# Kernel optimization log

Hardware: AMD Instinct MI355X
Metric: run time of the kernel (lower is better)

Reference implementation:

```python
import jax, jax.numpy as jnp
import numpy as np

NMS_THRE = 0.4
NEG = -1e30  # sentinel for sort key of suppressed boxes


def _iou_adjacency(boxes, nms_thre):
    # boxes: [N,4] in cxcywh -> xyxy, then dense IoU >= thre adjacency (no self loops)
    cx, cy, w, h = boxes[:, 0], boxes[:, 1], boxes[:, 2], boxes[:, 3]
    x1 = cx - w / 2
    y1 = cy - h / 2
    x2 = x1 + w
    y2 = y1 + h
    b = jnp.stack([x1, y1, x2, y2], axis=-1)  # [N,4]
    area = (x2 - x1) * (y2 - y1)
    lt = jnp.maximum(b[:, None, :2], b[None, :, :2])  # [N,N,2]
    rb = jnp.minimum(b[:, None, 2:], b[None, :, 2:])
    wh = jnp.clip(rb - lt, 0.0)
    inter = wh[..., 0] * wh[..., 1]
    iou = inter / (area[:, None] + area[None, :] - inter)
    n = boxes.shape[0]
    return (iou >= nms_thre) & (~jnp.eye(n, dtype=bool))


def _greedy_suppress(valid0, adj, scores):
    # Sequential greedy NMS over candidates in descending score order.
    # valid shrinks monotonically, and valid <= valid0 always, so clearing
    # neighbors via adj row exactly matches the torch loop (which only clears
    # neighbors that were initially valid -- already-false entries are no-ops).
    order = jnp.argsort(-scores)

    def body(k, valid):
        idx = order[k]
        return jnp.where(valid[idx], valid & (~adj[idx]), valid)

    return jax.lax.fori_loop(0, scores.shape[0], body, valid0)


def _per_class(pro_c, con_c, conf_c, adj):
    # scatter_max over adjacency: max of con over neighbors (0 if no neighbors,
    # matching torch_scatter's zero-init)
    adj_con = jnp.max(jnp.where(adj, con_c[None, :], 0.0), axis=1)
    valid0 = (pro_c >= conf_c) & (pro_c >= adj_con) & (pro_c >= con_c)
    return _greedy_suppress(valid0, adj, pro_c)


def _per_image(pro, con, boxes, scale, conf_thres):
    # pro/con: [N,C]; boxes: [N,4] cxcywh; scale: scalar; conf_thres: [C]
    adj = _iou_adjacency(boxes, NMS_THRE)
    survive = jax.vmap(_per_class, in_axes=(1, 1, 0, None))(pro, con, conf_thres, adj)  # [C,N]
    b = boxes * scale
    cx, cy, w, h = b[:, 0], b[:, 1], b[:, 2], b[:, 3]
    xyxy = jnp.stack([cx - 0.5 * w, cy - 0.5 * h, cx + 0.5 * w, cy + 0.5 * h], axis=-1)  # [N,4]
    scores = pro.T  # [C,N]
    C = scores.shape[0]
    bws = jnp.concatenate(
        [jnp.broadcast_to(xyxy[None], (C,) + xyxy.shape), scores[..., None]], axis=-1
    )  # [C,N,5]
    bws = bws * survive[..., None].astype(bws.dtype)  # zero out suppressed rows
    key = jnp.where(survive, scores, NEG)
    perm = jnp.argsort(-key, axis=1)  # per-class descending score order
    bws = jnp.take_along_axis(bws, perm[..., None], axis=1)
    mask = jnp.take_along_axis(survive, perm, axis=1)
    return bws, mask


def setup_inputs() -> dict:
    key = jax.random.key(0)
    k1, k2, k3, k4 = jax.random.split(key, 4)
    B, N, C = 4, 3600, 16
    return {
        "pro_max": jax.random.uniform(k1, (B, N, C), dtype=jnp.float32),
        "con_max": jax.random.uniform(k2, (B, N, C), dtype=jnp.float32),
        "pred_boxes": jax.random.uniform(k3, (B, N, 4), dtype=jnp.float32),
        "image_scales": jax.random.uniform(k4, (B,), dtype=jnp.float32),
        "conf_thres": jnp.zeros((C,), dtype=jnp.float32),
    }


def reference(pro_max, con_max, pred_boxes, image_scales, conf_thres):
    # Returns (boxes_with_scores [B,C,N,5] sorted per class by score desc,
    #          survive_mask [B,C,N] aligned with the sorted rows).
    return jax.vmap(_per_image, in_axes=(0, 0, 0, 0, None))(
        pro_max, con_max, pred_boxes, image_scales, conf_thres
    )
```

## Files before the change

kernel.cpp:

```cpp
#include <hip/hip_runtime.h>
#include <cstdint>

typedef unsigned long long u64;
typedef unsigned int u32;

#define B_ 4
#define N_ 3600
#define C_ 16
#define NW_ 57
#define NPAD_ 3648
#define RPW_ 4
#define RPB_ 16
#define TPI_ 1596
#define HW0_ 1856
#define HW1_ 1792
#define CH_ 64
#define NT_ 512
#define NWV_ 8
#define RPWG_ 8

__global__ __launch_bounds__(256, 4) void k_adj(const float* __restrict__ boxes,
                                                u64* __restrict__ adj) {
#pragma clang fp contract(off)
    __shared__ float4 sbox[HW0_];
    const int tid  = threadIdx.x;
    const int lane = tid & 63;
    const int wv   = tid >> 6;
    const int g    = blockIdx.x;
    const int b    = g / (N_ / RPB_);
    const int rg   = g % (N_ / RPB_);
    const int r0   = rg * RPB_ + wv * RPW_;
    const int w0   = rg >> 2;
    const size_t bN = (size_t)b * N_;

    float4 bi[RPW_];
    float  ai[RPW_];
#pragma unroll
    for (int r = 0; r < RPW_; ++r) {
        const float4 bx = reinterpret_cast<const float4*>(boxes)[bN + r0 + r];
        const float x1 = bx.x - bx.z * 0.5f;
        const float y1 = bx.y - bx.w * 0.5f;
        const float x2 = x1 + bx.z;
        const float y2 = y1 + bx.w;
        bi[r] = make_float4(x1, y1, x2, y2);
        ai[r] = (x2 - x1) * (y2 - y1);
    }
    const double MID = (double)0.4f - 0x1p-26;

    u64 row[RPW_];
#pragma unroll
    for (int r = 0; r < RPW_; ++r) row[r] = 0ull;

    int jbase = 0;
    for (int h = 0; h < 2; ++h) {
        const int cnt  = h ? HW1_ : HW0_;
        const int wlo  = jbase >> 6;
        const int wcnt = cnt >> 6;
        if (w0 < wlo + wcnt) {
            const int tw0 = max(w0 - wlo, 0);
            const int jj0 = tw0 << 6;
            __syncthreads();
            for (int jj = jj0 + tid; jj < cnt; jj += 256) {
                const int j = jbase + jj;
                float x1 = 0.f, y1 = 0.f, x2 = 0.f, y2 = 0.f;
                if (j < N_) {
                    const float4 bx = reinterpret_cast<const float4*>(boxes)[bN + j];
                    x1 = bx.x - bx.z * 0.5f;
                    y1 = bx.y - bx.w * 0.5f;
                    x2 = x1 + bx.z;
                    y2 = y1 + bx.w;
                }
                sbox[jj] = make_float4(x1, y1, x2, y2);
            }
            __syncthreads();

            for (int tw = tw0; tw < wcnt; ++tw) {
                const int tglob = wlo + tw;
                const float4 bj = sbox[tw * 64 + lane];
                const float ajr = (bj.z - bj.x) * (bj.w - bj.y);
#pragma unroll
                for (int r = 0; r < RPW_; ++r) {
                    const float ltx = fmaxf(bi[r].x, bj.x);
                    const float lty = fmaxf(bi[r].y, bj.y);
                    const float rbx = fminf(bi[r].z, bj.z);
                    const float rby = fminf(bi[r].w, bj.w);
                    const float whx = fmaxf(rbx - ltx, 0.0f);
                    const float why = fmaxf(rby - lty, 0.0f);
                    const float inter = whx * why;
                    const float denom = (ai[r] + ajr) - inter;
                    const int pred = ((double)inter > MID * (double)denom);
                    const u64 m = __ballot(pred);
                    if (lane == tglob) row[r] = m;
                }
            }
        }
        jbase += cnt;
    }

#pragma unroll
    for (int r = 0; r < RPW_; ++r)
        if (lane == w0) row[r] &= ~(1ull << ((r0 + r) & 63));

#pragma unroll
    for (int r = 0; r < RPW_; ++r)
        if (lane >= w0 && lane < NW_)
            adj[(bN + r0 + r) * (size_t)NW_ + lane] = row[r];
}

__global__ __launch_bounds__(256) void k_tr(u64* __restrict__ adj,
                                            u32* __restrict__ cnt) {
    if (blockIdx.x == 0) {
        for (int x = threadIdx.x; x < B_ * C_ * 16; x += 256) cnt[x] = 0;
    }
    const int lane = threadIdx.x & 63;
    const int wv   = threadIdx.x >> 6;
    const int p    = blockIdx.x * 4 + wv;
    const int b    = p / TPI_;
    const int p2   = p % TPI_;
    int wi = (int)((1.0f + sqrtf((float)(8 * p2 + 1))) * 0.5f);
    while (wi * (wi - 1) / 2 > p2) --wi;
    while ((wi + 1) * wi / 2 <= p2) ++wi;
    const int wj = p2 - wi * (wi - 1) / 2;
    const size_t bN = (size_t)b * N_;

    u64 x = adj[(bN + wj * 64 + lane) * (size_t)NW_ + wi];

    const u64 M[6] = {0x00000000FFFFFFFFull, 0x0000FFFF0000FFFFull,
                      0x00FF00FF00FF00FFull, 0x0F0F0F0F0F0F0F0Full,
                      0x3333333333333333ull, 0x5555555555555555ull};
#pragma unroll
    for (int si = 0; si < 6; ++si) {
        const int s = 32 >> si;
        const u64 m = M[si];
        const u64 t = __shfl_xor(x, s);
        x = ((lane & s) == 0) ? ((x & m) | ((t & m) << s))
                              : ((x & ~m) | ((t & ~m) >> s));
    }

    const int rowi = wi * 64 + lane;
    if (rowi < N_)
        adj[(bN + rowi) * (size_t)NW_ + wj] = x;
}

__global__ __launch_bounds__(256) void k_acon(const u64* __restrict__ adj,
                                              const float* __restrict__ con,
                                              const float* __restrict__ pro,
                                              const float* __restrict__ conf,
                                              u64* __restrict__ cand,
                                              u32* __restrict__ cnt) {
    const int tid  = threadIdx.x;
    const int lane = tid & 63;
    const int wv   = tid >> 6;
    const int g    = blockIdx.x;
    const int b    = g / (N_ / 4);
    const int i    = (g % (N_ / 4)) * 4 + wv;
    const size_t bN = (size_t)b * N_;

    u64 w = (lane < NW_) ? adj[(bN + i) * (size_t)NW_ + lane] : 0ull;

    float cm[C_];
#pragma unroll
    for (int k = 0; k < C_; ++k) cm[k] = 0.0f;

    while (w) {
        const int bit = __builtin_ctzll(w); w &= w - 1;
        const int j   = lane * 64 + bit;
        const float4* cp = reinterpret_cast<const float4*>(con + (bN + j) * C_);
        const float4 c0 = cp[0], c1 = cp[1], c2 = cp[2], c3 = cp[3];
        cm[0]  = fmaxf(cm[0],  c0.x); cm[1]  = fmaxf(cm[1],  c0.y);
        cm[2]  = fmaxf(cm[2],  c0.z); cm[3]  = fmaxf(cm[3],  c0.w);
        cm[4]  = fmaxf(cm[4],  c1.x); cm[5]  = fmaxf(cm[5],  c1.y);
        cm[6]  = fmaxf(cm[6],  c1.z); cm[7]  = fmaxf(cm[7],  c1.w);
        cm[8]  = fmaxf(cm[8],  c2.x); cm[9]  = fmaxf(cm[9],  c2.y);
        cm[10] = fmaxf(cm[10], c2.z); cm[11] = fmaxf(cm[11], c2.w);
        cm[12] = fmaxf(cm[12], c3.x); cm[13] = fmaxf(cm[13], c3.y);
        cm[14] = fmaxf(cm[14], c3.z); cm[15] = fmaxf(cm[15], c3.w);
    }

#pragma unroll
    for (int off = 1; off < 64; off <<= 1) {
#pragma unroll
        for (int k = 0; k < C_; ++k) cm[k] = fmaxf(cm[k], __shfl_xor(cm[k], off));
    }
    if (lane == 0) {
        const float4* cp = reinterpret_cast<const float4*>(con + (bN + i) * C_);
        const float4 c0 = cp[0], c1 = cp[1], c2 = cp[2], c3 = cp[3];
        const float4* pp = reinterpret_cast<const float4*>(pro + (bN + i) * C_);
        const float4 p0 = pp[0], p1 = pp[1], p2 = pp[2], p3 = pp[3];
        const float4* fp = reinterpret_cast<const float4*>(conf);
        const float4 f0 = fp[0], f1 = fp[1], f2 = fp[2], f3 = fp[3];
        const float th[C_] = {
            fmaxf(cm[0],  c0.x), fmaxf(cm[1],  c0.y),
            fmaxf(cm[2],  c0.z), fmaxf(cm[3],  c0.w),
            fmaxf(cm[4],  c1.x), fmaxf(cm[5],  c1.y),
            fmaxf(cm[6],  c1.z), fmaxf(cm[7],  c1.w),
            fmaxf(cm[8],  c2.x), fmaxf(cm[9],  c2.y),
            fmaxf(cm[10], c2.z), fmaxf(cm[11], c2.w),
            fmaxf(cm[12], c3.x), fmaxf(cm[13], c3.y),
            fmaxf(cm[14], c3.z), fmaxf(cm[15], c3.w)};
        const float pr[C_] = {p0.x, p0.y, p0.z, p0.w, p1.x, p1.y, p1.z, p1.w,
                              p2.x, p2.y, p2.z, p2.w, p3.x, p3.y, p3.z, p3.w};
        const float cf[C_] = {f0.x, f0.y, f0.z, f0.w, f1.x, f1.y, f1.z, f1.w,
                              f2.x, f2.y, f2.z, f2.w, f3.x, f3.y, f3.z, f3.w};
#pragma unroll
        for (int k = 0; k < C_; ++k) {
            if (pr[k] >= cf[k] && pr[k] >= th[k]) {
                const u32 pb = __float_as_uint(pr[k]);
                const u32 pk = pb ^ ((pb >> 31) ? 0xFFFFFFFFu : 0x80000000u);
                const u32 pos = atomicAdd(&cnt[(b * C_ + k) * 16], 1u);
                cand[(size_t)(b * C_ + k) * N_ + pos] =
                    (((u64)(~pk)) << 32) | (u32)i;
            }
        }
    }
}

union OvT {
    u64 keys[NPAD_];
    u64 srows[2][CH_][NW_];
};

__global__ __launch_bounds__(NT_) void k_nms(const u64* __restrict__ cand,
                                             const u32* __restrict__ cnt,
                                             const u64* __restrict__ adj,
                                             const float* __restrict__ boxes,
                                             const float* __restrict__ scales,
                                             float* __restrict__ out) {
#pragma clang fp contract(off)
    __shared__ OvT ov;
    __shared__ u32 sidx[NPAD_];
    __shared__ float sscore[NPAD_];
    __shared__ u64 sintra[CH_];
    __shared__ u64 vmask[NW_];
    __shared__ u64 s_accept;
    __shared__ u32 slist[NPAD_];
    __shared__ float slistf[NPAD_];
    __shared__ u32 s_S;
    const int tid  = threadIdx.x;
    const int lane = tid & 63;
    const int wv   = tid >> 6;
    const int bc   = blockIdx.x;
    const int b    = bc / C_;
    const size_t bN = (size_t)b * N_;

    const int T  = (int)cnt[bc * 16];
    const int TW = (T + 63) >> 6;
    for (int x = tid; x < TW * 64; x += NT_)
        ov.keys[x] = (x < T) ? cand[(size_t)bc * N_ + x] : ~0ull;
    if (tid < NW_) vmask[tid] = 0ull;
    __syncthreads();

    for (int xp = 0; xp * NT_ < T; ++xp) {
        const int x  = xp * NT_ + tid;
        const u64 kx = (x < T) ? ov.keys[x] : ~0ull;
        u32 rank = 0;
        for (int yb = 0; yb < TW; ++yb) {
            const u64 ky = ov.keys[yb * 64 + lane];
            const u32 kyl = (u32)ky, kyh = (u32)(ky >> 32);
#pragma unroll
            for (int l = 0; l < 64; ++l) {
                const u64 kb =
                    ((u64)(u32)__builtin_amdgcn_readlane((int)kyh, l) << 32)
                  |  (u64)(u32)__builtin_amdgcn_readlane((int)kyl, l);
                rank += (kb < kx) ? 1u : 0u;
            }
        }
        if (x < T) {
            const u32 i = (u32)(kx & 0xFFFFFFFFull);
            sidx[rank] = i;
            const u32 pk = ~((u32)(kx >> 32));
            const u32 pb = (pk & 0x80000000u) ? (pk ^ 0x80000000u) : ~pk;
            sscore[rank] = __uint_as_float(pb);
            atomicOr(&vmask[i >> 6], 1ull << (i & 63));
        }
    }
    __syncthreads();

#pragma unroll
    for (int rr = 0; rr < RPWG_; ++rr) {
        const int r = wv * RPWG_ + rr;
        const u32 idx = (r < T) ? sidx[r] : 0u;
        if (lane < NW_) ov.srows[0][r][lane] = adj[(bN + idx) * (size_t)NW_ + lane];
    }
    __syncthreads();

    u32 S = 0;
    const int NCH = (T + CH_ - 1) / CH_;
    for (int ch = 0; ch < NCH; ++ch) {
        const int cur = ch & 1, nxt = cur ^ 1;
        const int c0 = ch * CH_;
        const int cn = min(CH_, T - c0);
        const int havenext = (ch + 1 < NCH);

        u64 pre[RPWG_];
#pragma unroll
        for (int rr = 0; rr < RPWG_; ++rr) {
            const int r = wv * RPWG_ + rr;
            const int q = c0 + CH_ + r;
            const u32 idxn = (havenext && q < T) ? sidx[q] : 0u;
            pre[rr] = (havenext && lane < NW_)
                        ? adj[(bN + idxn) * (size_t)NW_ + lane] : 0ull;
        }
#pragma unroll
        for (int rr = 0; rr < RPWG_; ++rr) {
            const int r = wv * RPWG_ + rr;
            const u32 idxr = (c0 + r < T) ? sidx[c0 + r] : 0u;
            const u64 rj = ov.srows[cur][lane][idxr >> 6];
            const u64 ib = __ballot((lane < cn) && ((rj >> (idxr & 63)) & 1ull));
            if (lane == 0) sintra[r] = ib;
        }
        __syncthreads();

        if (wv == 0) {
            const u32 idxme = (c0 + lane < T) ? sidx[c0 + lane] : 0u;
            const u64 vm = vmask[idxme >> 6];
            u64 cv = __ballot((lane < cn) && ((vm >> (idxme & 63)) & 1ull));
            const u64 iv = sintra[lane];
            const u32 ivLo = (u32)iv, ivHi = (u32)(iv >> 32);
            u64 accept = 0ull;
            while (cv) {
                const int r = __builtin_ctzll(cv);
                accept |= 1ull << r;
                const u64 ir =
                    ((u64)(u32)__builtin_amdgcn_readlane((int)ivHi, r) << 32)
                  |  (u64)(u32)__builtin_amdgcn_readlane((int)ivLo, r);
                cv &= ~(ir | (1ull << r));
            }
            if (lane == 0) s_accept = accept;
            const u32 bitl = (u32)((accept >> lane) & 1ull);
            if (bitl) {
                const u32 pos = S + (u32)__popcll(accept & ((1ull << lane) - 1ull));
                slist[pos]  = idxme;
                slistf[pos] = sscore[c0 + lane];
            }
            S += (u32)__popcll(accept);
        }
        __syncthreads();

        const u64 ac = s_accept;
        u64 acc = 0ull;
#pragma unroll
        for (int rr = 0; rr < RPWG_; ++rr) {
            const int r = wv * RPWG_ + rr;
            if ((ac >> r) & 1ull)
                acc |= ov.srows[cur][r][min(lane, NW_ - 1)];
        }
        if (lane < NW_ && acc)
            atomicAnd(&vmask[lane], ~acc);
        if (havenext) {
#pragma unroll
            for (int rr = 0; rr < RPWG_; ++rr) {
                const int r = wv * RPWG_ + rr;
                if (lane < NW_) ov.srows[nxt][r][lane] = pre[rr];
            }
        }
        __syncthreads();
    }
    if (wv == 0 && lane == 0) s_S = S;
    __syncthreads();

    const int Sf = (int)s_S;
    const float s = scales[b];
    for (int r = tid; r < N_; r += NT_) {
        float o0 = 0.f, o1 = 0.f, o2 = 0.f, o3 = 0.f, o4 = 0.f, mk = 0.f;
        if (r < Sf) {
            const int idx = (int)slist[r];
            const float4 bx = reinterpret_cast<const float4*>(boxes)[bN + idx];
            const float scx = bx.x * s, scy = bx.y * s;
            const float sw  = bx.z * s, sh  = bx.w * s;
            o0 = scx - 0.5f * sw;
            o1 = scy - 0.5f * sh;
            o2 = scx + 0.5f * sw;
            o3 = scy + 0.5f * sh;
            o4 = slistf[r];
            mk = 1.0f;
        }
        float* o = out + ((size_t)bc * N_ + r) * 5;
        o[0] = o0; o[1] = o1; o[2] = o2; o[3] = o3; o[4] = o4;
        out[(size_t)B_ * C_ * N_ * 5 + (size_t)bc * N_ + r] = mk;
    }
}

extern "C" void kernel_launch(void* const* d_in, const int* in_sizes, int n_in,
                              void* d_out, int out_size, void* d_ws, size_t ws_size,
                              hipStream_t stream) {
    const float* pro    = (const float*)d_in[0];
    const float* con    = (const float*)d_in[1];
    const float* boxes  = (const float*)d_in[2];
    const float* scales = (const float*)d_in[3];
    const float* conf   = (const float*)d_in[4];

    char* ws = (char*)d_ws;
    u64* adj = (u64*)ws;
    size_t off = (size_t)B_ * N_ * NW_ * sizeof(u64);
    u64* cand = (u64*)(ws + off);
    off += (size_t)B_ * C_ * N_ * sizeof(u64);
    u32* cnt = (u32*)(ws + off);

    k_adj <<<B_ * N_ / RPB_, 256, 0, stream>>>(boxes, adj);
    k_tr  <<<B_ * TPI_ / 4,  256, 0, stream>>>(adj, cnt);
    k_acon<<<B_ * N_ / 4,    256, 0, stream>>>(adj, con, pro, conf, cand, cnt);
    k_nms <<<B_ * C_,        NT_, 0, stream>>>(cand, cnt, adj, boxes,
                                               scales, (float*)d_out);
}
```

Baseline: 170.7 us.

## Fuse four NMS kernels into one cooperative persistent kernel with grid syncs

Merges the adjacency, transpose, neighbor-max/candidate and greedy NMS kernels into a single cooperative launch of 256 persistent blocks separated by grid.sync, removing launch gaps between stages. The output is pre-zeroed up front so the final stage writes only surviving rows. The intra-chunk greedy acceptance loop now resolves several non-conflicting candidates per iteration using ballot and an OR-reduction instead of one readlane step per candidate. Costs include grid-wide barriers, lower parallelism in the early stages (256 blocks), and only 64 of the 256 blocks doing the serial NMS stage.

Measured after the change: 278.6 us. 1.63x slower.

```diff
diff --git a/kernel.cpp b/kernel.cpp
--- a/kernel.cpp
+++ b/kernel.cpp
@@ -1,5 +1,8 @@
 #include <hip/hip_runtime.h>
+#include <hip/hip_cooperative_groups.h>
 #include <cstdint>
+
+namespace cg = cooperative_groups;
 
 typedef unsigned long long u64;
 typedef unsigned int u32;
@@ -9,8 +12,9 @@
 #define C_ 16
 #define NW_ 57
 #define NPAD_ 3648
-#define RPW_ 4
+#define RPW_ 2
 #define RPB_ 16
+#define NUNITS_ (B_ * N_ / RPB_)
 #define TPI_ 1596
 #define HW0_ 1856
 #define HW1_ 1792
@@ -18,244 +22,257 @@
 #define NT_ 512
 #define NWV_ 8
 #define RPWG_ 8
-
-__global__ __launch_bounds__(256, 4) void k_adj(const float* __restrict__ boxes,
-                                                u64* __restrict__ adj) {
+#define GRID_ 256
+
+union SMem {
+    float4 sbox[HW0_];
+    struct {
+        union {
+            u64 keys[NPAD_];
+            u64 srows[2][CH_][NW_];
+        } ov;
+        u32 sidx[NPAD_];
+        float sscore[NPAD_];
+        u32 slist[NPAD_];
+        float slistf[NPAD_];
+        u64 sintra[CH_];
+        u64 vmask[NW_];
+        u64 s_accept;
+        u32 s_S;
+    } nms;
+};
+
+__global__ void __launch_bounds__(NT_) k_all(const float* __restrict__ pro,
+                                             const float* __restrict__ con,
+                                             const float* __restrict__ boxes,
+                                             const float* __restrict__ scales,
+                                             const float* __restrict__ conf,
+                                             u64* __restrict__ adj,
+                                             u64* __restrict__ cand,
+                                             u32* __restrict__ cnt,
+                                             float* __restrict__ out,
+                                             int nout) {
 #pragma clang fp contract(off)
-    __shared__ float4 sbox[HW0_];
+    __shared__ SMem sm;
+    cg::grid_group grid = cg::this_grid();
     const int tid  = threadIdx.x;
     const int lane = tid & 63;
     const int wv   = tid >> 6;
-    const int g    = blockIdx.x;
-    const int b    = g / (N_ / RPB_);
-    const int rg   = g % (N_ / RPB_);
-    const int r0   = rg * RPB_ + wv * RPW_;
-    const int w0   = rg >> 2;
-    const size_t bN = (size_t)b * N_;
-
-    float4 bi[RPW_];
-    float  ai[RPW_];
-#pragma unroll
-    for (int r = 0; r < RPW_; ++r) {
-        const float4 bx = reinterpret_cast<const float4*>(boxes)[bN + r0 + r];
-        const float x1 = bx.x - bx.z * 0.5f;
-        const float y1 = bx.y - bx.w * 0.5f;
-        const float x2 = x1 + bx.z;
-        const float y2 = y1 + bx.w;
-        bi[r] = make_float4(x1, y1, x2, y2);
-        ai[r] = (x2 - x1) * (y2 - y1);
-    }
+    const int bid  = blockIdx.x;
     const double MID = (double)0.4f - 0x1p-26;
 
-    u64 row[RPW_];
-#pragma unroll
-    for (int r = 0; r < RPW_; ++r) row[r] = 0ull;
-
-    int jbase = 0;
-    for (int h = 0; h < 2; ++h) {
-        const int cnt  = h ? HW1_ : HW0_;
-        const int wlo  = jbase >> 6;
-        const int wcnt = cnt >> 6;
-        if (w0 < wlo + wcnt) {
-            const int tw0 = max(w0 - wlo, 0);
-            const int jj0 = tw0 << 6;
-            __syncthreads();
-            for (int jj = jj0 + tid; jj < cnt; jj += 256) {
-                const int j = jbase + jj;
-                float x1 = 0.f, y1 = 0.f, x2 = 0.f, y2 = 0.f;
-                if (j < N_) {
-                    const float4 bx = reinterpret_cast<const float4*>(boxes)[bN + j];
-                    x1 = bx.x - bx.z * 0.5f;
-                    y1 = bx.y - bx.w * 0.5f;
-                    x2 = x1 + bx.z;
-                    y2 = y1 + bx.w;
+    {
+        float4* o4 = reinterpret_cast<float4*>(out);
+        const int n4 = nout >> 2;
+        const float4 z = make_float4(0.f, 0.f, 0.f, 0.f);
+        for (int x = bid * NT_ + tid; x < n4; x += GRID_ * NT_) o4[x] = z;
+        if (bid == 0)
+            for (int x = tid; x < B_ * C_ * 16; x += NT_) cnt[x] = 0;
+    }
+
+    for (int u = bid; u < NUNITS_; u += GRID_) {
+        const int b  = u / (N_ / RPB_);
+        const int rg = u % (N_ / RPB_);
+        const int r0 = rg * RPB_ + wv * RPW_;
+        const int w0 = rg >> 2;
+        const size_t bN = (size_t)b * N_;
+
+        float4 bi[RPW_];
+        float  ai[RPW_];
+#pragma unroll
+        for (int r = 0; r < RPW_; ++r) {
+            const float4 bx = reinterpret_cast<const float4*>(boxes)[bN + r0 + r];
+            const float x1 = bx.x - bx.z * 0.5f;
+            const float y1 = bx.y - bx.w * 0.5f;
+            const float x2 = x1 + bx.z;
+            const float y2 = y1 + bx.w;
+            bi[r] = make_float4(x1, y1, x2, y2);
+            ai[r] = (x2 - x1) * (y2 - y1);
+        }
+
+        u64 row[RPW_];
+#pragma unroll
+        for (int r = 0; r < RPW_; ++r) row[r] = 0ull;
+
+        int jbase = 0;
+        for (int h = 0; h < 2; ++h) {
+            const int cnt_h = h ? HW1_ : HW0_;
+            const int wlo   = jbase >> 6;
+            const int wcnt  = cnt_h >> 6;
+            if (w0 < wlo + wcnt) {
+                const int tw0 = max(w0 - wlo, 0);
+                const int jj0 = tw0 << 6;
+                __syncthreads();
+                for (int jj = jj0 + tid; jj < cnt_h; jj += NT_) {
+                    const int j = jbase + jj;
+                    float x1 = 0.f, y1 = 0.f, x2 = 0.f, y2 = 0.f;
+                    if (j < N_) {
+                        const float4 bx =
+                            reinterpret_cast<const float4*>(boxes)[bN + j];
+                        x1 = bx.x - bx.z * 0.5f;
+                        y1 = bx.y - bx.w * 0.5f;
+                        x2 = x1 + bx.z;
+                        y2 = y1 + bx.w;
+                    }
+                    sm.sbox[jj] = make_float4(x1, y1, x2, y2);
                 }
-                sbox[jj] = make_float4(x1, y1, x2, y2);
-            }
-            __syncthreads();
-
-            for (int tw = tw0; tw < wcnt; ++tw) {
-                const int tglob = wlo + tw;
-                const float4 bj = sbox[tw * 64 + lane];
-                const float ajr = (bj.z - bj.x) * (bj.w - bj.y);
-#pragma unroll
-                for (int r = 0; r < RPW_; ++r) {
-                    const float ltx = fmaxf(bi[r].x, bj.x);
-                    const float lty = fmaxf(bi[r].y, bj.y);
-                    const float rbx = fminf(bi[r].z, bj.z);
-                    const float rby = fminf(bi[r].w, bj.w);
-                    const float whx = fmaxf(rbx - ltx, 0.0f);
-                    const float why = fmaxf(rby - lty, 0.0f);
-                    const float inter = whx * why;
-                    const float denom = (ai[r] + ajr) - inter;
-                    const int pred = ((double)inter > MID * (double)denom);
-                    const u64 m = __ballot(pred);
-                    if (lane == tglob) row[r] = m;
+                __syncthreads();
+
+                for (int tw = tw0; tw < wcnt; ++tw) {
+                    const int tglob = wlo + tw;
+                    const float4 bj = sm.sbox[tw * 64 + lane];
+                    const float ajr = (bj.z - bj.x) * (bj.w - bj.y);
+#pragma unroll
+                    for (int r = 0; r < RPW_; ++r) {
+                        const float ltx = fmaxf(bi[r].x, bj.x);
+                        const float lty = fmaxf(bi[r].y, bj.y);
+                        const float rbx = fminf(bi[r].z, bj.z);
+                        const float rby = fminf(bi[r].w, bj.w);
+                        const float whx = fmaxf(rbx - ltx, 0.0f);
+                        const float why = fmaxf(rby - lty, 0.0f);
+                        const float inter = whx * why;
+                        const float denom = (ai[r] + ajr) - inter;
+                        const int pred = ((double)inter > MID * (double)denom);
+                        const u64 m = __ballot(pred);
+                        if (lane == tglob) row[r] = m;
+                    }
                 }
             }
-        }
-        jbase += cnt;
-    }
-
-#pragma unroll
-    for (int r = 0; r < RPW_; ++r)
-        if (lane == w0) row[r] &= ~(1ull << ((r0 + r) & 63));
-
-#pragma unroll
-    for (int r = 0; r < RPW_; ++r)
-        if (lane >= w0 && lane < NW_)
-            adj[(bN + r0 + r) * (size_t)NW_ + lane] = row[r];
-}
-
-__global__ __launch_bounds__(256) void k_tr(u64* __restrict__ adj,
-                                            u32* __restrict__ cnt) {
-    if (blockIdx.x == 0) {
-        for (int x = threadIdx.x; x < B_ * C_ * 16; x += 256) cnt[x] = 0;
-    }
-    const int lane = threadIdx.x & 63;
-    const int wv   = threadIdx.x >> 6;
-    const int p    = blockIdx.x * 4 + wv;
-    const int b    = p / TPI_;
-    const int p2   = p % TPI_;
-    int wi = (int)((1.0f + sqrtf((float)(8 * p2 + 1))) * 0.5f);
-    while (wi * (wi - 1) / 2 > p2) --wi;
-    while ((wi + 1) * wi / 2 <= p2) ++wi;
-    const int wj = p2 - wi * (wi - 1) / 2;
-    const size_t bN = (size_t)b * N_;
-
-    u64 x = adj[(bN + wj * 64 + lane) * (size_t)NW_ + wi];
-
-    const u64 M[6] = {0x00000000FFFFFFFFull, 0x0000FFFF0000FFFFull,
-                      0x00FF00FF00FF00FFull, 0x0F0F0F0F0F0F0F0Full,
-                      0x3333333333333333ull, 0x5555555555555555ull};
-#pragma unroll
-    for (int si = 0; si < 6; ++si) {
-        const int s = 32 >> si;
-        const u64 m = M[si];
-        const u64 t = __shfl_xor(x, s);
-        x = ((lane & s) == 0) ? ((x & m) | ((t & m) << s))
-                              : ((x & ~m) | ((t & ~m) >> s));
-    }
-
-    const int rowi = wi * 64 + lane;
-    if (rowi < N_)
-        adj[(bN + rowi) * (size_t)NW_ + wj] = x;
-}
-
-__global__ __launch_bounds__(256) void k_acon(const u64* __restrict__ adj,
-                                              const float* __restrict__ con,
-                                              const float* __restrict__ pro,
-                                              const float* __restrict__ conf,
-                                              u64* __restrict__ cand,
-                                              u32* __restrict__ cnt) {
-    const int tid  = threadIdx.x;
-    const int lane = tid & 63;
-    const int wv   = tid >> 6;
-    const int g    = blockIdx.x;
-    const int b    = g / (N_ / 4);
-    const int i    = (g % (N_ / 4)) * 4 + wv;
-    const size_t bN = (size_t)b * N_;
-
-    u64 w = (lane < NW_) ? adj[(bN + i) * (size_t)NW_ + lane] : 0ull;
-
-    float cm[C_];
-#pragma unroll
-    for (int k = 0; k < C_; ++k) cm[k] = 0.0f;
-
-    while (w) {
-        const int bit = __builtin_ctzll(w); w &= w - 1;
-        const int j   = lane * 64 + bit;
-        const float4* cp = reinterpret_cast<const float4*>(con + (bN + j) * C_);
-        const float4 c0 = cp[0], c1 = cp[1], c2 = cp[2], c3 = cp[3];
-        cm[0]  = fmaxf(cm[0],  c0.x); cm[1]  = fmaxf(cm[1],  c0.y);
-        cm[2]  = fmaxf(cm[2],  c0.z); cm[3]  = fmaxf(cm[3],  c0.w);
-        cm[4]  = fmaxf(cm[4],  c1.x); cm[5]  = fmaxf(cm[5],  c1.y);
-        cm[6]  = fmaxf(cm[6],  c1.z); cm[7]  = fmaxf(cm[7],  c1.w);
-        cm[8]  = fmaxf(cm[8],  c2.x); cm[9]  = fmaxf(cm[9],  c2.y);
-        cm[10] = fmaxf(cm[10], c2.z); cm[11] = fmaxf(cm[11], c2.w);
-        cm[12] = fmaxf(cm[12], c3.x); cm[13] = fmaxf(cm[13], c3.y);
-        cm[14] = fmaxf(cm[14], c3.z); cm[15] = fmaxf(cm[15], c3.w);
-    }
-
-#pragma unroll
-    for (int off = 1; off < 64; off <<= 1) {
-#pragma unroll
-        for (int k = 0; k < C_; ++k) cm[k] = fmaxf(cm[k], __shfl_xor(cm[k], off));
-    }
-    if (lane == 0) {
-        const float4* cp = reinterpret_cast<const float4*>(con + (bN + i) * C_);
-        const float4 c0 = cp[0], c1 = cp[1], c2 = cp[2], c3 = cp[3];
-        const float4* pp = reinterpret_cast<const float4*>(pro + (bN + i) * C_);
-        const float4 p0 = pp[0], p1 = pp[1], p2 = pp[2], p3 = pp[3];
-        const float4* fp = reinterpret_cast<const float4*>(conf);
-        const float4 f0 = fp[0], f1 = fp[1], f2 = fp[2], f3 = fp[3];
-        const float th[C_] = {
-            fmaxf(cm[0],  c0.x), fmaxf(cm[1],  c0.y),
-            fmaxf(cm[2],  c0.z), fmaxf(cm[3],  c0.w),
-            fmaxf(cm[4],  c1.x), fmaxf(cm[5],  c1.y),
-            fmaxf(cm[6],  c1.z), fmaxf(cm[7],  c1.w),
-            fmaxf(cm[8],  c2.x), fmaxf(cm[9],  c2.y),
-            fmaxf(cm[10], c2.z), fmaxf(cm[11], c2.w),
-            fmaxf(cm[12], c3.x), fmaxf(cm[13], c3.y),
-            fmaxf(cm[14], c3.z), fmaxf(cm[15], c3.w)};
-        const float pr[C_] = {p0.x, p0.y, p0.z, p0.w, p1.x, p1.y, p1.z, p1.w,
-                              p2.x, p2.y, p2.z, p2.w, p3.x, p3.y, p3.z, p3.w};
-        const float cf[C_] = {f0.x, f0.y, f0.z, f0.w, f1.x, f1.y, f1.z, f1.w,
-                              f2.x, f2.y, f2.z, f2.w, f3.x, f3.y, f3.z, f3.w};
-#pragma unroll
-        for (int k = 0; k < C_; ++k) {
-            if (pr[k] >= cf[k] && pr[k] >= th[k]) {
-                const u32 pb = __float_as_uint(pr[k]);
-                const u32 pk = pb ^ ((pb >> 31) ? 0xFFFFFFFFu : 0x80000000u);
-                const u32 pos = atomicAdd(&cnt[(b * C_ + k) * 16], 1u);
-                cand[(size_t)(b * C_ + k) * N_ + pos] =
-                    (((u64)(~pk)) << 32) | (u32)i;
-            }
-        }
-    }
-}
-
-union OvT {
-    u64 keys[NPAD_];
-    u64 srows[2][CH_][NW_];
-};
-
-__global__ __launch_bounds__(NT_) void k_nms(const u64* __restrict__ cand,
-                                             const u32* __restrict__ cnt,
-                                             const u64* __restrict__ adj,
-                                             const float* __restrict__ boxes,
-                                             const float* __restrict__ scales,
-                                             float* __restrict__ out) {
-#pragma clang fp contract(off)
-    __shared__ OvT ov;
-    __shared__ u32 sidx[NPAD_];
-    __shared__ float sscore[NPAD_];
-    __shared__ u64 sintra[CH_];
-    __shared__ u64 vmask[NW_];
-    __shared__ u64 s_accept;
-    __shared__ u32 slist[NPAD_];
-    __shared__ float slistf[NPAD_];
-    __shared__ u32 s_S;
-    const int tid  = threadIdx.x;
-    const int lane = tid & 63;
-    const int wv   = tid >> 6;
-    const int bc   = blockIdx.x;
-    const int b    = bc / C_;
+            jbase += cnt_h;
+        }
+
+#pragma unroll
+        for (int r = 0; r < RPW_; ++r)
+            if (lane == w0) row[r] &= ~(1ull << ((r0 + r) & 63));
+#pragma unroll
+        for (int r = 0; r < RPW_; ++r)
+            if (lane >= w0 && lane < NW_)
+                adj[(bN + r0 + r) * (size_t)NW_ + lane] = row[r];
+    }
+
+    grid.sync();
+
+    for (int p = bid * NWV_ + wv; p < B_ * TPI_; p += GRID_ * NWV_) {
+        const int b  = p / TPI_;
+        const int p2 = p % TPI_;
+        int wi = (int)((1.0f + sqrtf((float)(8 * p2 + 1))) * 0.5f);
+        while (wi * (wi - 1) / 2 > p2) --wi;
+        while ((wi + 1) * wi / 2 <= p2) ++wi;
+        const int wj = p2 - wi * (wi - 1) / 2;
+        const size_t bN = (size_t)b * N_;
+
+        u64 x = adj[(bN + wj * 64 + lane) * (size_t)NW_ + wi];
+
+        const u64 M[6] = {0x00000000FFFFFFFFull, 0x0000FFFF0000FFFFull,
+                          0x00FF00FF00FF00FFull, 0x0F0F0F0F0F0F0F0Full,
+                          0x3333333333333333ull, 0x5555555555555555ull};
+#pragma unroll
+        for (int si = 0; si < 6; ++si) {
+            const int s = 32 >> si;
+            const u64 m = M[si];
+            const u64 t = __shfl_xor(x, s);
+            x = ((lane & s) == 0) ? ((x & m) | ((t & m) << s))
+                                  : ((x & ~m) | ((t & ~m) >> s));
+        }
+        const int rowi = wi * 64 + lane;
+        if (rowi < N_)
+            adj[(bN + rowi) * (size_t)NW_ + wj] = x;
+    }
+
+    grid.sync();
+
+    for (int g = bid * NWV_ + wv; g < B_ * N_; g += GRID_ * NWV_) {
+        const int b = g / N_;
+        const int i = g % N_;
+        const size_t bN = (size_t)b * N_;
+
+        u64 w = (lane < NW_) ? adj[(bN + i) * (size_t)NW_ + lane] : 0ull;
+
+        float cm[C_];
+#pragma unroll
+        for (int k = 0; k < C_; ++k) cm[k] = 0.0f;
+
+        while (w) {
+            const int bit = __builtin_ctzll(w); w &= w - 1;
+            const int j   = lane * 64 + bit;
+            const float4* cp =
+                reinterpret_cast<const float4*>(con + (bN + j) * C_);
+            const float4 c0 = cp[0], c1 = cp[1], c2 = cp[2], c3 = cp[3];
+            cm[0]  = fmaxf(cm[0],  c0.x); cm[1]  = fmaxf(cm[1],  c0.y);
+            cm[2]  = fmaxf(cm[2],  c0.z); cm[3]  = fmaxf(cm[3],  c0.w);
+            cm[4]  = fmaxf(cm[4],  c1.x); cm[5]  = fmaxf(cm[5],  c1.y);
+            cm[6]  = fmaxf(cm[6],  c1.z); cm[7]  = fmaxf(cm[7],  c1.w);
+            cm[8]  = fmaxf(cm[8],  c2.x); cm[9]  = fmaxf(cm[9],  c2.y);
+            cm[10] = fmaxf(cm[10], c2.z); cm[11] = fmaxf(cm[11], c2.w);
+            cm[12] = fmaxf(cm[12], c3.x); cm[13] = fmaxf(cm[13], c3.y);
+            cm[14] = fmaxf(cm[14], c3.z); cm[15] = fmaxf(cm[15], c3.w);
+        }
+
+#pragma unroll
+        for (int off = 1; off < 64; off <<= 1) {
+#pragma unroll
+            for (int k = 0; k < C_; ++k)
+                cm[k] = fmaxf(cm[k], __shfl_xor(cm[k], off));
+        }
+        if (lane == 0) {
+            const float4* cp =
+                reinterpret_cast<const float4*>(con + (bN + i) * C_);
+            const float4 c0 = cp[0], c1 = cp[1], c2 = cp[2], c3 = cp[3];
+            const float4* pp =
+                reinterpret_cast<const float4*>(pro + (bN + i) * C_);
+            const float4 p0 = pp[0], p1 = pp[1], p2 = pp[2], p3 = pp[3];
+            const float4* fp = reinterpret_cast<const float4*>(conf);
+            const float4 f0 = fp[0], f1 = fp[1], f2 = fp[2], f3 = fp[3];
+            const float th[C_] = {
+                fmaxf(cm[0],  c0.x), fmaxf(cm[1],  c0.y),
+                fmaxf(cm[2],  c0.z), fmaxf(cm[3],  c0.w),
+                fmaxf(cm[4],  c1.x), fmaxf(cm[5],  c1.y),
+                fmaxf(cm[6],  c1.z), fmaxf(cm[7],  c1.w),
+                fmaxf(cm[8],  c2.x), fmaxf(cm[9],  c2.y),
+                fmaxf(cm[10], c2.z), fmaxf(cm[11], c2.w),
+                fmaxf(cm[12], c3.x), fmaxf(cm[13], c3.y),
+                fmaxf(cm[14], c3.z), fmaxf(cm[15], c3.w)};
+            const float pr[C_] = {p0.x, p0.y, p0.z, p0.w,
+                                  p1.x, p1.y, p1.z, p1.w,
+                                  p2.x, p2.y, p2.z, p2.w,
+                                  p3.x, p3.y, p3.z, p3.w};
+            const float cf[C_] = {f0.x, f0.y, f0.z, f0.w,
+                                  f1.x, f1.y, f1.z, f1.w,
+                                  f2.x, f2.y, f2.z, f2.w,
+                                  f3.x, f3.y, f3.z, f3.w};
+#pragma unroll
+            for (int k = 0; k < C_; ++k) {
+                if (pr[k] >= cf[k] && pr[k] >= th[k]) {
+                    const u32 pb = __float_as_uint(pr[k]);
+                    const u32 pk = pb ^ ((pb >> 31) ? 0xFFFFFFFFu : 0x80000000u);
+                    const u32 pos = atomicAdd(&cnt[(b * C_ + k) * 16], 1u);
+                    cand[(size_t)(b * C_ + k) * N_ + pos] =
+                        (((u64)(~pk)) << 32) | (u32)i;
+                }
+            }
+        }
+    }
+
+    grid.sync();
+
+    if (bid >= B_ * C_) return;
+    const int bc = bid;
+    const int b  = bc / C_;
     const size_t bN = (size_t)b * N_;
 
     const int T  = (int)cnt[bc * 16];
     const int TW = (T + 63) >> 6;
     for (int x = tid; x < TW * 64; x += NT_)
-        ov.keys[x] = (x < T) ? cand[(size_t)bc * N_ + x] : ~0ull;
-    if (tid < NW_) vmask[tid] = 0ull;
+        sm.nms.ov.keys[x] = (x < T) ? cand[(size_t)bc * N_ + x] : ~0ull;
+    if (tid < NW_) sm.nms.vmask[tid] = 0ull;
     __syncthreads();
 
     for (int xp = 0; xp * NT_ < T; ++xp) {
         const int x  = xp * NT_ + tid;
-        const u64 kx = (x < T) ? ov.keys[x] : ~0ull;
+        const u64 kx = (x < T) ? sm.nms.ov.keys[x] : ~0ull;
         u32 rank = 0;
         for (int yb = 0; yb < TW; ++yb) {
-            const u64 ky = ov.keys[yb * 64 + lane];
+            const u64 ky = sm.nms.ov.keys[yb * 64 + lane];
             const u32 kyl = (u32)ky, kyh = (u32)(ky >> 32);
 #pragma unroll
             for (int l = 0; l < 64; ++l) {
@@ -267,11 +284,11 @@
         }
         if (x < T) {
             const u32 i = (u32)(kx & 0xFFFFFFFFull);
-            sidx[rank] = i;
+            sm.nms.sidx[rank] = i;
             const u32 pk = ~((u32)(kx >> 32));
             const u32 pb = (pk & 0x80000000u) ? (pk ^ 0x80000000u) : ~pk;
-            sscore[rank] = __uint_as_float(pb);
-            atomicOr(&vmask[i >> 6], 1ull << (i & 63));
+            sm.nms.sscore[rank] = __uint_as_float(pb);
+            atomicOr(&sm.nms.vmask[i >> 6], 1ull << (i & 63));
         }
     }
     __syncthreads();
@@ -279,8 +296,9 @@
 #pragma unroll
     for (int rr = 0; rr < RPWG_; ++rr) {
         const int r = wv * RPWG_ + rr;
-        const u32 idx = (r < T) ? sidx[r] : 0u;
-        if (lane < NW_) ov.srows[0][r][lane] = adj[(bN + idx) * (size_t)NW_ + lane];
+        const u32 idx = (r < T) ? sm.nms.sidx[r] : 0u;
+        if (lane < NW_)
+            sm.nms.ov.srows[0][r][lane] = adj[(bN + idx) * (size_t)NW_ + lane];
     }
     __syncthreads();
 
@@ -297,87 +315,84 @@
         for (int rr = 0; rr < RPWG_; ++rr) {
             const int r = wv * RPWG_ + rr;
             const int q = c0 + CH_ + r;
-            const u32 idxn = (havenext && q < T) ? sidx[q] : 0u;
+            const u32 idxn = (havenext && q < T) ? sm.nms.sidx[q] : 0u;
             pre[rr] = (havenext && lane < NW_)
                         ? adj[(bN + idxn) * (size_t)NW_ + lane] : 0ull;
         }
 #pragma unroll
         for (int rr = 0; rr < RPWG_; ++rr) {
             const int r = wv * RPWG_ + rr;
-            const u32 idxr = (c0 + r < T) ? sidx[c0 + r] : 0u;
-            const u64 rj = ov.srows[cur][lane][idxr >> 6];
+            const u32 idxr = (c0 + r < T) ? sm.nms.sidx[c0 + r] : 0u;
+            const u64 rj = sm.nms.ov.srows[cur][lane][idxr >> 6];
             const u64 ib = __ballot((lane < cn) && ((rj >> (idxr & 63)) & 1ull));
-            if (lane == 0) sintra[r] = ib;
+            if (lane == 0) sm.nms.sintra[r] = ib;
         }
         __syncthreads();
 
         if (wv == 0) {
-            const u32 idxme = (c0 + lane < T) ? sidx[c0 + lane] : 0u;
-            const u64 vm = vmask[idxme >> 6];
+            const u32 idxme = (c0 + lane < T) ? sm.nms.sidx[c0 + lane] : 0u;
+            const u64 vm = sm.nms.vmask[idxme >> 6];
             u64 cv = __ballot((lane < cn) && ((vm >> (idxme & 63)) & 1ull));
-            const u64 iv = sintra[lane];
-            const u32 ivLo = (u32)iv, ivHi = (u32)(iv >> 32);
+            const u64 iv = sm.nms.sintra[lane];
+            const u64 below = (1ull << lane) - 1ull;
             u64 accept = 0ull;
             while (cv) {
-                const int r = __builtin_ctzll(cv);
-                accept |= 1ull << r;
-                const u64 ir =
-                    ((u64)(u32)__builtin_amdgcn_readlane((int)ivHi, r) << 32)
-                  |  (u64)(u32)__builtin_amdgcn_readlane((int)ivLo, r);
-                cv &= ~(ir | (1ull << r));
-            }
-            if (lane == 0) s_accept = accept;
-            const u32 bitl = (u32)((accept >> lane) & 1ull);
-            if (bitl) {
-                const u32 pos = S + (u32)__popcll(accept & ((1ull << lane) - 1ull));
-                slist[pos]  = idxme;
-                slistf[pos] = sscore[c0 + lane];
+                const int ok = ((cv >> lane) & 1ull) &&
+                               ((iv & below & cv) == 0ull);
+                const u64 ar = __ballot(ok);
+                u64 sup = ok ? iv : 0ull;
+#pragma unroll
+                for (int off = 1; off < 64; off <<= 1)
+                    sup |= __shfl_xor(sup, off);
+                accept |= ar;
+                cv &= ~(ar | sup);
+            }
+            if (lane == 0) sm.nms.s_accept = accept;
+            if ((accept >> lane) & 1ull) {
+                const u32 pos = S + (u32)__popcll(accept & below);
+                sm.nms.slist[pos]  = idxme;
+                sm.nms.slistf[pos] = sm.nms.sscore[c0 + lane];
             }
             S += (u32)__popcll(accept);
         }
         __syncthreads();
 
-        const u64 ac = s_accept;
+        const u64 ac = sm.nms.s_accept;
         u64 acc = 0ull;
 #pragma unroll
         for (int rr = 0; rr < RPWG_; ++rr) {
             const int r = wv * RPWG_ + rr;
             if ((ac >> r) & 1ull)
-                acc |= ov.srows[cur][r][min(lane, NW_ - 1)];
+                acc |= sm.nms.ov.srows[cur][r][min(lane, NW_ - 1)];
         }
         if (lane < NW_ && acc)
-            atomicAnd(&vmask[lane], ~acc);
+            atomicAnd(&sm.nms.vmask[lane], ~acc);
         if (havenext) {
 #pragma unroll
             for (int rr = 0; rr < RPWG_; ++rr) {
                 const int r = wv * RPWG_ + rr;
-                if (lane < NW_) ov.srows[nxt][r][lane] = pre[rr];
+                if (lane < NW_) sm.nms.ov.srows[nxt][r][lane] = pre[rr];
             }
         }
         __syncthreads();
     }
-    if (wv == 0 && lane == 0) s_S = S;
+    if (wv == 0 && lane == 0) sm.nms.s_S = S;
     __syncthreads();
 
-    const int Sf = (int)s_S;
+    const int Sf = (int)sm.nms.s_S;
     const float s = scales[b];
-    for (int r = tid; r < N_; r += NT_) {
-        float o0 = 0.f, o1 = 0.f, o2 = 0.f, o3 = 0.f, o4 = 0.f, mk = 0.f;
-        if (r < Sf) {
-            const int idx = (int)slist[r];
-            const float4 bx = reinterpret_cast<const float4*>(boxes)[bN + idx];
-            const float scx = bx.x * s, scy = bx.y * s;
-            const float sw  = bx.z * s, sh  = bx.w * s;
-            o0 = scx - 0.5f * sw;
-            o1 = scy - 0.5f * sh;
-            o2 = scx + 0.5f * sw;
-            o3 = scy + 0.5f * sh;
-            o4 = slistf[r];
-            mk = 1.0f;
-        }
+    for (int r = tid; r < Sf; r += NT_) {
+        const int idx = (int)sm.nms.slist[r];
+        const float4 bx = reinterpret_cast<const float4*>(boxes)[bN + idx];
+        const float scx = bx.x * s, scy = bx.y * s;
+        const float sw  = bx.z * s, sh  = bx.w * s;
         float* o = out + ((size_t)bc * N_ + r) * 5;
-        o[0] = o0; o[1] = o1; o[2] = o2; o[3] = o3; o[4] = o4;
-        out[(size_t)B_ * C_ * N_ * 5 + (size_t)bc * N_ + r] = mk;
+        o[0] = scx - 0.5f * sw;
+        o[1] = scy - 0.5f * sh;
+        o[2] = scx + 0.5f * sw;
+        o[3] = scy + 0.5f * sh;
+        o[4] = sm.nms.slistf[r];
+        out[(size_t)B_ * C_ * N_ * 5 + (size_t)bc * N_ + r] = 1.0f;
     }
 }
 
@@ -397,9 +412,11 @@
     off += (size_t)B_ * C_ * N_ * sizeof(u64);
     u32* cnt = (u32*)(ws + off);
 
-    k_adj <<<B_ * N_ / RPB_, 256, 0, stream>>>(boxes, adj);
-    k_tr  <<<B_ * TPI_ / 4,  256, 0, stream>>>(adj, cnt);
-    k_acon<<<B_ * N_ / 4,    256, 0, stream>>>(adj, con, pro, conf, cand, cnt);
-    k_nms <<<B_ * C_,        NT_, 0, stream>>>(cand, cnt, adj, boxes,
-                                               scales, (float*)d_out);
+    float* outp = (float*)d_out;
+    int nout = out_size;
+    void* args[] = {(void*)&pro, (void*)&con, (void*)&boxes, (void*)&scales,
+                    (void*)&conf, (void*)&adj, (void*)&cand, (void*)&cnt,
+                    (void*)&outp, (void*)&nout};
+    hipLaunchCooperativeKernel((const void*)k_all, dim3(GRID_), dim3(NT_),
+                               args, 0, stream);
 }
```

## Add compact candidate-space NMS kernel for small candidate counts with parallel intra-chunk resolve

Applied to the files above, without the earlier changes.

Adds a fast NMS kernel used when a (batch,class) has at most 512 candidates. It builds a compact candidate-by-candidate adjacency matrix in shared memory and tracks validity as bitmasks over candidate ranks instead of global box indices. The intra-chunk greedy resolve in both kernels becomes a parallel fixed-point iteration, accepting every candidate with no unsuppressed higher-ranked neighbour each round, replacing the serial per-candidate loop. The original kernel remains as a fallback that exits early for small counts, which costs an extra launch.

Result: slower. 197.8 us (+15.9%).

```diff
diff --git a/kernel.cpp b/kernel.cpp
--- a/kernel.cpp
+++ b/kernel.cpp
@@ -18,6 +18,9 @@
 #define NT_ 512
 #define NWV_ 8
 #define RPWG_ 8
+#define TMAX_ 512
+#define TWMX_ 8
+#define CPAD_ 9
 
 __global__ __launch_bounds__(256, 4) void k_adj(const float* __restrict__ boxes,
                                                 u64* __restrict__ adj) {
@@ -100,7 +103,6 @@
 #pragma unroll
     for (int r = 0; r < RPW_; ++r)
         if (lane == w0) row[r] &= ~(1ull << ((r0 + r) & 63));
-
 #pragma unroll
     for (int r = 0; r < RPW_; ++r)
         if (lane >= w0 && lane < NW_)
@@ -136,7 +138,6 @@
         x = ((lane & s) == 0) ? ((x & m) | ((t & m) << s))
                               : ((x & ~m) | ((t & ~m) >> s));
     }
-
     const int rowi = wi * 64 + lane;
     if (rowi < N_)
         adj[(bN + rowi) * (size_t)NW_ + wj] = x;
@@ -215,17 +216,156 @@
     }
 }
 
+__global__ __launch_bounds__(NT_) void k_nms_fast(const u64* __restrict__ cand,
+                                                  const u32* __restrict__ cnt,
+                                                  const u64* __restrict__ adj,
+                                                  const float* __restrict__ boxes,
+                                                  const float* __restrict__ scales,
+                                                  float* __restrict__ out) {
+#pragma clang fp contract(off)
+    __shared__ union {
+        u64 keys[TMAX_];
+        u64 cmat[TMAX_][CPAD_];
+    } ov;
+    __shared__ u32 sidx[TMAX_];
+    __shared__ float sscore[TMAX_];
+    __shared__ u32 slist[TMAX_];
+    __shared__ float slistf[TMAX_];
+    __shared__ u64 valid[TWMX_];
+    __shared__ u64 s_accept;
+    __shared__ u32 s_S;
+    const int tid  = threadIdx.x;
+    const int lane = tid & 63;
+    const int wv   = tid >> 6;
+    const int bc   = blockIdx.x;
+    const int b    = bc / C_;
+    const size_t bN = (size_t)b * N_;
+
+    const int T = (int)cnt[bc * 16];
+    if (T > TMAX_) return;
+    const int TW = (T + 63) >> 6;
+
+    for (int x = tid; x < TW * 64; x += NT_)
+        ov.keys[x] = (x < T) ? cand[(size_t)bc * N_ + x] : ~0ull;
+    if (tid < TWMX_) valid[tid] = ~0ull;
+    __syncthreads();
+
+    {
+        const u64 kx = (tid < T) ? ov.keys[tid] : ~0ull;
+        u32 rank = 0;
+        for (int yb = 0; yb < TW; ++yb) {
+            const u64 ky = ov.keys[yb * 64 + lane];
+            const u32 kyl = (u32)ky, kyh = (u32)(ky >> 32);
+#pragma unroll
+            for (int l = 0; l < 64; ++l) {
+                const u64 kb =
+                    ((u64)(u32)__builtin_amdgcn_readlane((int)kyh, l) << 32)
+                  |  (u64)(u32)__builtin_amdgcn_readlane((int)kyl, l);
+                rank += (kb < kx) ? 1u : 0u;
+            }
+        }
+        if (tid < T) {
+            sidx[rank] = (u32)(kx & 0xFFFFFFFFull);
+            const u32 pk = ~((u32)(kx >> 32));
+            const u32 pb = (pk & 0x80000000u) ? (pk ^ 0x80000000u) : ~pk;
+            sscore[rank] = __uint_as_float(pb);
+        }
+        for (int x = T + tid; x < TW * 64; x += NT_) sidx[x] = 0u;
+    }
+    __syncthreads();
+
+    for (int r = wv; r < T; r += NWV_) {
+        const u32 ir = sidx[r];
+        const u64 w = (lane < NW_) ? adj[(bN + ir) * (size_t)NW_ + lane] : 0ull;
+        for (int g = 0; g < TW; ++g) {
+            const u32 jc = sidx[g * 64 + lane];
+            const u64 wj = __shfl(w, (int)(jc >> 6));
+            const u64 bm = __ballot((wj >> (jc & 63)) & 1ull);
+            if (lane == 0) ov.cmat[r][g] = bm;
+        }
+    }
+    __syncthreads();
+
+    u32 S = 0;
+    const int NCH = (T + CH_ - 1) / CH_;
+    for (int ch = 0; ch < NCH; ++ch) {
+        const int c0 = ch * CH_;
+        const int cn = min(CH_, T - c0);
+
+        if (wv == 0) {
+            const u64 cmask = (cn >= 64) ? ~0ull : ((1ull << cn) - 1ull);
+            u64 cv = valid[ch] & cmask;
+            const u64 iv = (lane < cn) ? ov.cmat[c0 + lane][ch] : 0ull;
+            const u64 below = (1ull << lane) - 1ull;
+            u64 accept = 0ull;
+            while (cv) {
+                const int ok = ((cv >> lane) & 1ull) &&
+                               ((iv & below & cv) == 0ull);
+                const u64 ar = __ballot(ok);
+                u64 sup = ok ? iv : 0ull;
+#pragma unroll
+                for (int off = 1; off < 64; off <<= 1)
+                    sup |= __shfl_xor(sup, off);
+                accept |= ar;
+                cv &= ~(ar | sup);
+            }
+            if (lane == 0) s_accept = accept;
+            if ((accept >> lane) & 1ull) {
+                const u32 pos = S + (u32)__popcll(accept & below);
+                slist[pos]  = sidx[c0 + lane];
+                slistf[pos] = sscore[c0 + lane];
+            }
+            S += (u32)__popcll(accept);
+        }
+        __syncthreads();
+
+        const u64 ac = s_accept;
+        const int g = ch + 1 + wv;
+        if (g < TW && ac) {
+            u64 sup = ((ac >> lane) & 1ull) ? ov.cmat[c0 + lane][g] : 0ull;
+#pragma unroll
+            for (int off = 1; off < 64; off <<= 1)
+                sup |= __shfl_xor(sup, off);
+            if (lane == 0) valid[g] &= ~sup;
+        }
+        __syncthreads();
+    }
+    if (wv == 0 && lane == 0) s_S = S;
+    __syncthreads();
+
+    const int Sf = (int)s_S;
+    const float s = scales[b];
+    for (int r = tid; r < N_; r += NT_) {
+        float o0 = 0.f, o1 = 0.f, o2 = 0.f, o3 = 0.f, o4 = 0.f, mk = 0.f;
+        if (r < Sf) {
+            const int idx = (int)slist[r];
+            const float4 bx = reinterpret_cast<const float4*>(boxes)[bN + idx];
+            const float scx = bx.x * s, scy = bx.y * s;
+            const float sw  = bx.z * s, sh  = bx.w * s;
+            o0 = scx - 0.5f * sw;
+            o1 = scy - 0.5f * sh;
+            o2 = scx + 0.5f * sw;
+            o3 = scy + 0.5f * sh;
+            o4 = slistf[r];
+            mk = 1.0f;
+        }
+        float* o = out + ((size_t)bc * N_ + r) * 5;
+        o[0] = o0; o[1] = o1; o[2] = o2; o[3] = o3; o[4] = o4;
+        out[(size_t)B_ * C_ * N_ * 5 + (size_t)bc * N_ + r] = mk;
+    }
+}
+
 union OvT {
     u64 keys[NPAD_];
     u64 srows[2][CH_][NW_];
 };
 
-__global__ __launch_bounds__(NT_) void k_nms(const u64* __restrict__ cand,
-                                             const u32* __restrict__ cnt,
-                                             const u64* __restrict__ adj,
-                                             const float* __restrict__ boxes,
-                                             const float* __restrict__ scales,
-                                             float* __restrict__ out) {
+__global__ __launch_bounds__(NT_) void k_nms_slow(const u64* __restrict__ cand,
+                                                  const u32* __restrict__ cnt,
+                                                  const u64* __restrict__ adj,
+                                                  const float* __restrict__ boxes,
+                                                  const float* __restrict__ scales,
+                                                  float* __restrict__ out) {
 #pragma clang fp contract(off)
     __shared__ OvT ov;
     __shared__ u32 sidx[NPAD_];
@@ -244,6 +384,7 @@
     const size_t bN = (size_t)b * N_;
 
     const int T  = (int)cnt[bc * 16];
+    if (T <= TMAX_) return;
     const int TW = (T + 63) >> 6;
     for (int x = tid; x < TW * 64; x += NT_)
         ov.keys[x] = (x < T) ? cand[(size_t)bc * N_ + x] : ~0ull;
@@ -280,7 +421,8 @@
     for (int rr = 0; rr < RPWG_; ++rr) {
         const int r = wv * RPWG_ + rr;
         const u32 idx = (r < T) ? sidx[r] : 0u;
-        if (lane < NW_) ov.srows[0][r][lane] = adj[(bN + idx) * (size_t)NW_ + lane];
+        if (lane < NW_)
+            ov.srows[0][r][lane] = adj[(bN + idx) * (size_t)NW_ + lane];
     }
     __syncthreads();
 
@@ -316,20 +458,22 @@
             const u64 vm = vmask[idxme >> 6];
             u64 cv = __ballot((lane < cn) && ((vm >> (idxme & 63)) & 1ull));
             const u64 iv = sintra[lane];
-            const u32 ivLo = (u32)iv, ivHi = (u32)(iv >> 32);
+            const u64 below = (1ull << lane) - 1ull;
             u64 accept = 0ull;
             while (cv) {
-                const int r = __builtin_ctzll(cv);
-                accept |= 1ull << r;
-                const u64 ir =
-                    ((u64)(u32)__builtin_amdgcn_readlane((int)ivHi, r) << 32)
-                  |  (u64)(u32)__builtin_amdgcn_readlane((int)ivLo, r);
-                cv &= ~(ir | (1ull << r));
+                const int ok = ((cv >> lane) & 1ull) &&
+                               ((iv & below & cv) == 0ull);
+                const u64 ar = __ballot(ok);
+                u64 sup = ok ? iv : 0ull;
+#pragma unroll
+                for (int off = 1; off < 64; off <<= 1)
+                    sup |= __shfl_xor(sup, off);
+                accept |= ar;
+                cv &= ~(ar | sup);
             }
             if (lane == 0) s_accept = accept;
-            const u32 bitl = (u32)((accept >> lane) & 1ull);
-            if (bitl) {
-                const u32 pos = S + (u32)__popcll(accept & ((1ull << lane) - 1ull));
+            if ((accept >> lane) & 1ull) {
+                const u32 pos = S + (u32)__popcll(accept & below);
                 slist[pos]  = idxme;
                 slistf[pos] = sscore[c0 + lane];
             }
@@ -397,9 +541,11 @@
     off += (size_t)B_ * C_ * N_ * sizeof(u64);
     u32* cnt = (u32*)(ws + off);
 
-    k_adj <<<B_ * N_ / RPB_, 256, 0, stream>>>(boxes, adj);
-    k_tr  <<<B_ * TPI_ / 4,  256, 0, stream>>>(adj, cnt);
-    k_acon<<<B_ * N_ / 4,    256, 0, stream>>>(adj, con, pro, conf, cand, cnt);
-    k_nms <<<B_ * C_,        NT_, 0, stream>>>(cand, cnt, adj, boxes,
-                                               scales, (float*)d_out);
+    k_adj     <<<B_ * N_ / RPB_, 256, 0, stream>>>(boxes, adj);
+    k_tr      <<<B_ * TPI_ / 4,  256, 0, stream>>>(adj, cnt);
+    k_acon    <<<B_ * N_ / 4,    256, 0, stream>>>(adj, con, pro, conf, cand, cnt);
+    k_nms_fast<<<B_ * C_,        NT_, 0, stream>>>(cand, cnt, adj, boxes,
+                                                   scales, (float*)d_out);
+    k_nms_slow<<<B_ * C_,        NT_, 0, stream>>>(cand, cnt, adj, boxes,
+                                                   scales, (float*)d_out);
 }
```
